# Kernel tuning notes

Measured on AMD Instinct MI355X. Metric: run time of the kernel, lower is better.

Reference implementation:

```python
import jax, jax.numpy as jnp
import numpy as np

H = 256          # decoder_size
V = 3            # vocab_size
MAX_LENGTH = 64


def lstm_cell(x, h, c, Wih, Whh, b):
    # PyTorch gate order: i, f, g, o
    g = x @ Wih.T + h @ Whh.T + b
    i, f, gg, o = jnp.split(g, 4, axis=-1)
    c = jax.nn.sigmoid(f) * c + jax.nn.sigmoid(i) * jnp.tanh(gg)
    h = jax.nn.sigmoid(o) * jnp.tanh(c)
    return h, c


def setup_inputs() -> dict:
    key = jax.random.key(0)
    ks = jax.random.split(key, 16)
    T, B, F = 512, 32, 1024
    s = 1.0 / np.sqrt(H)
    u = lambda k, shape: jax.random.uniform(k, shape, jnp.float32, -s, s)
    return dict(
        cnn_feats=jax.random.normal(ks[0], (T, B, F), jnp.float32),
        # bidirectional encoder LSTM (1 layer)
        enc_Wih_f=u(ks[1], (4 * H, F)), enc_Whh_f=u(ks[2], (4 * H, H)), enc_b_f=u(ks[3], (4 * H,)),
        enc_Wih_b=u(ks[4], (4 * H, F)), enc_Whh_b=u(ks[5], (4 * H, H)), enc_b_b=u(ks[6], (4 * H,)),
        # 2-layer decoder LSTM
        dec_Wih0=u(ks[7], (4 * H, H)), dec_Whh0=u(ks[8], (4 * H, H)), dec_b0=u(ks[9], (4 * H,)),
        dec_Wih1=u(ks[10], (4 * H, H)), dec_Whh1=u(ks[11], (4 * H, H)), dec_b1=u(ks[12], (4 * H,)),
        # per-step output projection
        lin_W=u(ks[13], (V, H)), lin_b=u(ks[14], (V,)),
    )


def _forward(cnn_feats, enc_Wih_f, enc_Whh_f, enc_b_f, enc_Wih_b, enc_Whh_b, enc_b_b,
             dec_Wih0, dec_Whh0, dec_b0, dec_Wih1, dec_Whh1, dec_b1, lin_W, lin_b):
    B = cnn_feats.shape[1]
    z = jnp.zeros((B, H), cnn_feats.dtype)

    def run_dir(seq, Wih, Whh, b):
        def step(carry, x):
            h, c = lstm_cell(x, carry[0], carry[1], Wih, Whh, b)
            return (h, c), None
        (h, c), _ = jax.lax.scan(step, (z, z), seq)
        return h, c

    # encoder final states: fwd over seq, bwd over reversed seq
    hf, cf = run_dir(cnn_feats, enc_Wih_f, enc_Whh_f, enc_b_f)
    hb, cb = run_dir(cnn_feats[::-1], enc_Wih_b, enc_Whh_b, enc_b_b)

    # decoder: layer0 init = fwd-dir state, layer1 init = bwd-dir state
    def dstep(carry, _):
        x, h0, c0, h1, c1 = carry
        h0, c0 = lstm_cell(x, h0, c0, dec_Wih0, dec_Whh0, dec_b0)
        h1, c1 = lstm_cell(h0, h1, c1, dec_Wih1, dec_Whh1, dec_b1)
        y = h1 @ lin_W.T + lin_b
        return (h1, h0, c0, h1, c1), y

    _, ys = jax.lax.scan(dstep, (z, hf, cf, hb, cb), None, length=MAX_LENGTH)
    return ys  # (MAX_LENGTH, B, V)


def reference(cnn_feats, enc_Wih_f, enc_Whh_f, enc_b_f, enc_Wih_b, enc_Whh_b, enc_b_b,
              dec_Wih0, dec_Whh0, dec_b0, dec_Wih1, dec_Whh1, dec_b1, lin_W, lin_b):
    return _forward(cnn_feats, enc_Wih_f, enc_Whh_f, enc_b_f, enc_Wih_b, enc_Whh_b, enc_b_b,
                    dec_Wih0, dec_Whh0, dec_b0, dec_Wih1, dec_Whh1, dec_b1, lin_W, lin_b)
```

## Files before the change

kernel.cpp:

```cpp
#include <hip/hip_runtime.h>
#include <stdint.h>
#include <stddef.h>

typedef __attribute__((ext_vector_type(8))) short  short8;
typedef __attribute__((ext_vector_type(4))) float  floatx4;
typedef unsigned long long u64;

#define SENT 0xAAAAAAAAAAAAAAAAull

static __device__ __forceinline__ float b2f(uint16_t h) {
  union { uint32_t u; float f; } v; v.u = ((uint32_t)h) << 16; return v.f;
}
static __device__ __forceinline__ uint16_t f2b(float f) {
  union { float f; uint32_t u; } v; v.f = f;
  uint32_t u = v.u;
  uint32_t r = u + 0x7FFFu + ((u >> 16) & 1u);
  return (uint16_t)(r >> 16);
}
static __device__ __forceinline__ float sigm(float x)  { return 1.0f / (1.0f + __expf(-x)); }
static __device__ __forceinline__ float tanh_f(float x){ return 1.0f - 2.0f / (1.0f + __expf(2.0f * x)); }

static __device__ __forceinline__ floatx4 mfma16(short8 a, short8 b, floatx4 c) {
  return __builtin_amdgcn_mfma_f32_16x16x32_bf16(a, b, c, 0, 0, 0);
}
static __device__ __forceinline__ short8 cvt8(const float* p) {
  short8 r;
  #pragma unroll
  for (int i = 0; i < 8; ++i) r[i] = (short)f2b(p[i]);
  return r;
}
static __device__ __forceinline__ u64 ld_h64(const u64* p) {
  return __hip_atomic_load(p, __ATOMIC_RELAXED, __HIP_MEMORY_SCOPE_AGENT);
}
static __device__ __forceinline__ void st_h64(uint16_t* p, u64 v) {
  __hip_atomic_store((u64*)p, v, __ATOMIC_RELAXED, __HIP_MEMORY_SCOPE_AGENT);
}
static __device__ __forceinline__ void poll8(const u64* p, u64* o) {
  for (;;) {
    bool ok = true;
    #pragma unroll
    for (int i = 0; i < 8; ++i) { o[i] = ld_h64(p + i); ok &= (o[i] != SENT); }
    if (ok) break;
    __builtin_amdgcn_s_sleep(1);
  }
}

#define H 256
#define FH 1024
#define BATCH 32
#define TSEQ 512
#define DSTEPS 64
#define ERING 8

__global__ __launch_bounds__(256) void gemm_xw(
    const float* __restrict__ A, const float* __restrict__ W,
    const float* __restrict__ bias, void* __restrict__ Cout, int out_f32)
{
  const int K = 1024, N = 1024;
  __shared__ uint16_t Ah[64 * 40], Al[64 * 40];
  __shared__ uint16_t Wh[64 * 40], Wl[64 * 40];
  const int m0 = blockIdx.x * 64;
  const int n0 = blockIdx.y * 64;
  const int tid = threadIdx.x;
  const int lane = tid & 63, w = tid >> 6;
  const int wm = w & 1, wn = w >> 1;
  const int l15 = lane & 15, q4 = lane >> 4;
  const int ldrow = tid >> 2, ldk = (tid & 3) * 8;

  floatx4 acc[2][2];
  for (int i = 0; i < 2; ++i) for (int j = 0; j < 2; ++j) acc[i][j] = (floatx4){0.f,0.f,0.f,0.f};

  for (int kb = 0; kb < K; kb += 32) {
    float aa[8], ww[8];
    {
      const float4* ap = (const float4*)(A + (size_t)(m0 + ldrow) * K + kb + ldk);
      const float4* wp = (const float4*)(W + (size_t)(n0 + ldrow) * K + kb + ldk);
      *(float4*)(aa) = ap[0]; *(float4*)(aa + 4) = ap[1];
      *(float4*)(ww) = wp[0]; *(float4*)(ww + 4) = wp[1];
    }
    short8 ah, al, wh, wl;
    #pragma unroll
    for (int i = 0; i < 8; ++i) {
      uint16_t h = f2b(aa[i]); ah[i] = (short)h; al[i] = (short)f2b(aa[i] - b2f(h));
      uint16_t g = f2b(ww[i]); wl[i] = (short)f2b(ww[i] - b2f(f2b(ww[i]) ? 0 : 0));
      wh[i] = (short)f2b(ww[i]); wl[i] = (short)f2b(ww[i] - b2f((uint16_t)wh[i]));
    }
    __syncthreads();
    *(short8*)(Ah + ldrow * 40 + ldk) = ah;
    *(short8*)(Al + ldrow * 40 + ldk) = al;
    *(short8*)(Wh + ldrow * 40 + ldk) = wh;
    *(short8*)(Wl + ldrow * 40 + ldk) = wl;
    __syncthreads();
    short8 afh[2], afl[2], bfh[2], bfl[2];
    #pragma unroll
    for (int mt = 0; mt < 2; ++mt) {
      afh[mt] = *(const short8*)(Ah + (wm * 32 + mt * 16 + l15) * 40 + q4 * 8);
      afl[mt] = *(const short8*)(Al + (wm * 32 + mt * 16 + l15) * 40 + q4 * 8);
    }
    #pragma unroll
    for (int nt = 0; nt < 2; ++nt) {
      bfh[nt] = *(const short8*)(Wh + (wn * 32 + nt * 16 + l15) * 40 + q4 * 8);
      bfl[nt] = *(const short8*)(Wl + (wn * 32 + nt * 16 + l15) * 40 + q4 * 8);
    }
    #pragma unroll
    for (int mt = 0; mt < 2; ++mt)
      #pragma unroll
      for (int nt = 0; nt < 2; ++nt) {
        acc[mt][nt] = mfma16(afh[mt], bfh[nt], acc[mt][nt]);
        acc[mt][nt] = mfma16(afh[mt], bfl[nt], acc[mt][nt]);
        acc[mt][nt] = mfma16(afl[mt], bfh[nt], acc[mt][nt]);
      }
  }
  #pragma unroll
  for (int mt = 0; mt < 2; ++mt)
    #pragma unroll
    for (int nt = 0; nt < 2; ++nt) {
      const int col = n0 + wn * 32 + nt * 16 + l15;
      const float bv = bias[col];
      #pragma unroll
      for (int r = 0; r < 4; ++r) {
        const int row = m0 + wm * 32 + mt * 16 + q4 * 4 + r;
        const float v = acc[mt][nt][r] + bv;
        if (out_f32) ((float*)Cout)[(size_t)row * N + col] = v;
        else         ((uint16_t*)Cout)[(size_t)row * N + col] = f2b(v);
      }
    }
}

__global__ __launch_bounds__(256, 1) void enc_rnn(
    const void* __restrict__ XgF, const void* __restrict__ XgB, int xg_f32,
    const float* __restrict__ WhhF, const float* __restrict__ WhhB,
    uint16_t* __restrict__ hslots,
    uint16_t* __restrict__ hfin, float* __restrict__ cfin)
{
  const int d = blockIdx.x >> 3, q = blockIdx.x & 7;
  const void*  Xg  = d ? XgB : XgF;
  const float* Whh = d ? WhhB : WhhF;
  uint16_t* hsl = hslots + d * (ERING * BATCH * H);
  const int jOff = q * 32;
  const int tid = threadIdx.x, lane = tid & 63, w = tid >> 6;
  const int tt = w & 1, nt = w >> 1, l15 = lane & 15, q4 = lane >> 4;
  const int b = nt * 16 + l15;
  const int jg = jOff + tt * 16 + q4 * 4;

  __shared__ uint16_t hS[2][32 * 264];
  __shared__ float    xgS[2][32 * 132];

  short8 Af[4][8];
  #pragma unroll
  for (int g = 0; g < 4; ++g) {
    const int grow = g * H + jOff + tt * 16 + l15;
    #pragma unroll
    for (int ks = 0; ks < 8; ++ks)
      Af[g][ks] = cvt8(Whh + (size_t)grow * H + ks * 32 + q4 * 8);
  }
  for (int i = tid; i < 32 * 264; i += 256) hS[0][i] = 0;

  float cc[4] = {0.f, 0.f, 0.f, 0.f};
  union HV { uint16_t u16[4]; u64 v; } hv; hv.v = 0ull;
  const int rb = tid >> 3, seg = tid & 7;
  const int cp = seg * 16;
  const int gge = cp >> 5, jj = cp & 31;

  for (int s = 0; s < TSEQ; ++s) {
    const int t = d ? (TSEQ - 1 - s) : s;
    const int p = s & 1;
    float xv[16];
    {
      const size_t base = (size_t)(t * BATCH + rb) * FH + gge * H + jOff + jj;
      if (xg_f32) {
        const float4* xs = (const float4*)((const float*)Xg + base);
        *(float4*)(xv) = xs[0]; *(float4*)(xv + 4) = xs[1];
        *(float4*)(xv + 8) = xs[2]; *(float4*)(xv + 12) = xs[3];
      } else {
        const uint16_t* xs = (const uint16_t*)Xg + base;
        #pragma unroll
        for (int i = 0; i < 16; ++i) xv[i] = b2f(xs[i]);
      }
    }

    if (s > 0) {
      u64 tmp[8];
      const u64* ps = (const u64*)(hsl + ((s - 1) & (ERING - 1)) * (BATCH * H) + rb * H + seg * 32);
      poll8(ps, tmp);
      #pragma unroll
      for (int i = 0; i < 8; ++i)
        *(u64*)(hS[p] + rb * 264 + seg * 32 + i * 4) = tmp[i];
    }
    if (s >= 2)
      st_h64(hsl + ((s - 2) & (ERING - 1)) * (BATCH * H) + b * H + jg, SENT);
    #pragma unroll
    for (int i = 0; i < 16; ++i) xgS[p][rb * 132 + cp + i] = xv[i];
    __syncthreads();

    floatx4 a0 = {0.f,0.f,0.f,0.f}, a1 = a0, a2 = a0, a3 = a0;
    #pragma unroll
    for (int ks = 0; ks < 8; ++ks) {
      short8 bfv = *(const short8*)(hS[p] + b * 264 + ks * 32 + q4 * 8);
      a0 = mfma16(Af[0][ks], bfv, a0);
      a1 = mfma16(Af[1][ks], bfv, a1);
      a2 = mfma16(Af[2][ks], bfv, a2);
      a3 = mfma16(Af[3][ks], bfv, a3);
    }
    #pragma unroll
    for (int r = 0; r < 4; ++r) {
      const int jl = tt * 16 + q4 * 4 + r;
      const float gi = a0[r] + xgS[p][b * 132 +      jl];
      const float gf = a1[r] + xgS[p][b * 132 + 32 + jl];
      const float gc = a2[r] + xgS[p][b * 132 + 64 + jl];
      const float go = a3[r] + xgS[p][b * 132 + 96 + jl];
      const float cn2 = sigm(gf) * cc[r] + sigm(gi) * tanh_f(gc);
      cc[r] = cn2;
      hv.u16[r] = f2b(sigm(go) * tanh_f(cn2));
    }
    st_h64(hsl + (s & (ERING - 1)) * (BATCH * H) + b * H + jg, hv.v);
  }
  #pragma unroll
  for (int r = 0; r < 4; ++r) {
    hfin[d * (BATCH * H) + b * H + jg + r] = hv.u16[r];
    cfin[d * (BATCH * H) + b * H + jg + r] = cc[r];
  }
}

__global__ __launch_bounds__(256, 1) void dec_rnn(
    const float* __restrict__ Wih0, const float* __restrict__ Whh0, const float* __restrict__ bb0,
    const float* __restrict__ Wih1, const float* __restrict__ Whh1, const float* __restrict__ bb1,
    const uint16_t* __restrict__ hfin, const float* __restrict__ cfin,
    uint16_t* __restrict__ h0slots,
    uint16_t* __restrict__ h1slots,
    float*    __restrict__ h1f)
{
  const int L = blockIdx.x >> 3, q = blockIdx.x & 7;
  const float* Wih = L ? Wih1 : Wih0;
  const float* Whh = L ? Whh1 : Whh0;
  const float* bs  = L ? bb1 : bb0;
  const int jOff = q * 32;
  const int tid = threadIdx.x, lane = tid & 63, w = tid >> 6;
  const int tt = w & 1, nt = w >> 1, l15 = lane & 15, q4 = lane >> 4;
  const int b = nt * 16 + l15;
  const int jg = jOff + tt * 16 + q4 * 4;

  __shared__ uint16_t xhS[2][32 * 528];

  short8 Af[4][16];
  #pragma unroll
  for (int g = 0; g < 4; ++g) {
    const int grow = g * H + jOff + tt * 16 + l15;
    #pragma unroll
    for (int ks = 0; ks < 8; ++ks) {
      Af[g][ks]     = cvt8(Wih + (size_t)grow * H + ks * 32 + q4 * 8);
      Af[g][8 + ks] = cvt8(Whh + (size_t)grow * H + ks * 32 + q4 * 8);
    }
  }
  float brg[4][4];
  #pragma unroll
  for (int g = 0; g < 4; ++g)
    #pragma unroll
    for (int r = 0; r < 4; ++r)
      brg[g][r] = bs[g * H + jOff + tt * 16 + q4 * 4 + r];

  float cc[4];
  #pragma unroll
  for (int r = 0; r < 4; ++r) cc[r] = cfin[L * (BATCH * H) + b * H + jg + r];

  const int rb = tid >> 3, seg = tid & 7;
  const size_t off = (size_t)rb * H + seg * 32;
  union HV { uint16_t u16[4]; u64 v; } hv; hv.v = 0ull;

  for (int t = 0; t < DSTEPS; ++t) {
    const int p = t & 1;
    u64 tx[8], th[8];
    if (t == 0) {
      const u64* ph = (const u64*)(hfin + L * (BATCH * H) + off);
      #pragma unroll
      for (int i = 0; i < 8; ++i) th[i] = ph[i];
    } else {
      const uint16_t* hb = (L ? h1slots : h0slots) + (size_t)(t - 1) * (BATCH * H);
      poll8((const u64*)(hb + off), th);
    }
    if (L == 0) {
      if (t == 0) {
        #pragma unroll
        for (int i = 0; i < 8; ++i) tx[i] = 0ull;
      } else {
        poll8((const u64*)(h1slots + (size_t)(t - 1) * (BATCH * H) + off), tx);
      }
    } else {
      poll8((const u64*)(h0slots + (size_t)t * (BATCH * H) + off), tx);
    }
    #pragma unroll
    for (int i = 0; i < 8; ++i) {
      *(u64*)(xhS[p] + rb * 528 + seg * 32 + i * 4) = tx[i];
      *(u64*)(xhS[p] + rb * 528 + 256 + seg * 32 + i * 4) = th[i];
    }
    __syncthreads();

    floatx4 a0 = {0.f,0.f,0.f,0.f}, a1 = a0, a2 = a0, a3 = a0;
    #pragma unroll
    for (int ks = 0; ks < 16; ++ks) {
      short8 bfv = *(const short8*)(xhS[p] + b * 528 + ks * 32 + q4 * 8);
      a0 = mfma16(Af[0][ks], bfv, a0);
      a1 = mfma16(Af[1][ks], bfv, a1);
      a2 = mfma16(Af[2][ks], bfv, a2);
      a3 = mfma16(Af[3][ks], bfv, a3);
    }
    float hval[4];
    #pragma unroll
    for (int r = 0; r < 4; ++r) {
      const float gi = a0[r] + brg[0][r];
      const float gf = a1[r] + brg[1][r];
      const float gc = a2[r] + brg[2][r];
      const float go = a3[r] + brg[3][r];
      const float cn2 = sigm(gf) * cc[r] + sigm(gi) * tanh_f(gc);
      cc[r] = cn2;
      hval[r] = sigm(go) * tanh_f(cn2);
      hv.u16[r] = f2b(hval[r]);
    }
    st_h64((L ? h1slots : h0slots) + (size_t)t * (BATCH * H) + b * H + jg, hv.v);
    if (L == 1) {
      float* df = h1f + (size_t)t * (BATCH * H) + b * H + jg;
      #pragma unroll
      for (int r = 0; r < 4; ++r) df[r] = hval[r];
    }
  }
}

__global__ __launch_bounds__(256) void out_proj(
    const float* __restrict__ h1f, const float* __restrict__ linW,
    const float* __restrict__ linb, float* __restrict__ out)
{
  const int idx = blockIdx.x * 256 + threadIdx.x;
  if (idx >= DSTEPS * BATCH * 3) return;
  const int v = idx % 3;
  const int tb = idx / 3;
  const float* hrow = h1f + (size_t)tb * H;
  const float* wrow = linW + (size_t)v * H;
  float s = linb[v];
  for (int k = 0; k < H; ++k) s += hrow[k] * wrow[k];
  out[idx] = s;
}

extern "C" void kernel_launch(void* const* d_in, const int* in_sizes, int n_in,
                              void* d_out, int out_size, void* d_ws, size_t ws_size,
                              hipStream_t stream) {
  (void)in_sizes; (void)n_in; (void)out_size;
  const float* cnn   = (const float*)d_in[0];
  const float* WihF  = (const float*)d_in[1];
  const float* WhhF  = (const float*)d_in[2];
  const float* bF    = (const float*)d_in[3];
  const float* WihB  = (const float*)d_in[4];
  const float* WhhB  = (const float*)d_in[5];
  const float* bB    = (const float*)d_in[6];
  const float* Wih0  = (const float*)d_in[7];
  const float* Whh0  = (const float*)d_in[8];
  const float* b0    = (const float*)d_in[9];
  const float* Wih1  = (const float*)d_in[10];
  const float* Whh1  = (const float*)d_in[11];
  const float* b1    = (const float*)d_in[12];
  const float* linW  = (const float*)d_in[13];
  const float* linb  = (const float*)d_in[14];

  const size_t XG_ELEMS = (size_t)TSEQ * BATCH * FH;
  const size_t SMALL = 2457600;
  const int xg_f32 = (ws_size >= 2 * XG_ELEMS * 4 + SMALL) ? 1 : 0;
  const size_t S = XG_ELEMS * (xg_f32 ? 4 : 2);

  uint8_t* ws = (uint8_t*)d_ws;
  void*     XgF    = (void*)(ws);
  void*     XgB    = (void*)(ws + S);
  float*    h1f    = (float*)(ws + S);
  uint8_t*  base   = ws + 2 * S;
  uint16_t* hslotsE = (uint16_t*)(base);
  uint16_t* h0slots = (uint16_t*)(base + 262144);
  uint16_t* h1slots = (uint16_t*)(base + 1310720);
  uint16_t* hfin    = (uint16_t*)(base + 2359296);
  float*    cfin    = (float*)(base + 2392064);

  hipMemsetAsync(base, 0xAA, 2359296, stream);

  gemm_xw<<<dim3(256, 16), 256, 0, stream>>>(cnn, WihF, bF, XgF, xg_f32);
  gemm_xw<<<dim3(256, 16), 256, 0, stream>>>(cnn, WihB, bB, XgB, xg_f32);
  enc_rnn<<<16, 256, 0, stream>>>(XgF, XgB, xg_f32, WhhF, WhhB,
                                  hslotsE, hfin, cfin);
  dec_rnn<<<16, 256, 0, stream>>>(Wih0, Whh0, b0, Wih1, Whh1, b1,
                                  hfin, cfin, h0slots, h1slots, h1f);
  out_proj<<<24, 256, 0, stream>>>(h1f, linW, linb, (float*)d_out);
}
```

Before: 2.589 ms.

## Co-locate recurrent blocks on one XCD and poll dual fast/slow h slots

```diff
diff --git a/kernel.cpp b/kernel.cpp
--- a/kernel.cpp
+++ b/kernel.cpp
@@ -4,6 +4,7 @@
 
 typedef __attribute__((ext_vector_type(8))) short  short8;
 typedef __attribute__((ext_vector_type(4))) float  floatx4;
+typedef __attribute__((ext_vector_type(4))) unsigned int uintx4;
 typedef unsigned long long u64;
 
 #define SENT 0xAAAAAAAAAAAAAAAAull
@@ -35,12 +36,45 @@
 static __device__ __forceinline__ void st_h64(uint16_t* p, u64 v) {
   __hip_atomic_store((u64*)p, v, __ATOMIC_RELAXED, __HIP_MEMORY_SCOPE_AGENT);
 }
-static __device__ __forceinline__ void poll8(const u64* p, u64* o) {
+static __device__ __forceinline__ void st64_sc0(uint16_t* p, u64 v) {
+  asm volatile("global_store_dwordx2 %0, %1, off sc0" : : "v"(p), "v"(v) : "memory");
+}
+static __device__ __forceinline__ void ld8_sc0(const u64* p, u64* o) {
+  uintx4 a, b, c, d;
+  asm volatile(
+    "global_load_dwordx4 %0, %4, off sc0\n\t"
+    "global_load_dwordx4 %1, %5, off sc0\n\t"
+    "global_load_dwordx4 %2, %6, off sc0\n\t"
+    "global_load_dwordx4 %3, %7, off sc0\n\t"
+    "s_waitcnt vmcnt(0)"
+    : "=&v"(a), "=&v"(b), "=&v"(c), "=&v"(d)
+    : "v"(p), "v"(p + 2), "v"(p + 4), "v"(p + 6)
+    : "memory");
+  o[0] = ((u64)a.y << 32) | a.x;  o[1] = ((u64)a.w << 32) | a.z;
+  o[2] = ((u64)b.y << 32) | b.x;  o[3] = ((u64)b.w << 32) | b.z;
+  o[4] = ((u64)c.y << 32) | c.x;  o[5] = ((u64)c.w << 32) | c.z;
+  o[6] = ((u64)d.y << 32) | d.x;  o[7] = ((u64)d.w << 32) | d.z;
+}
+static __device__ __forceinline__ void poll8_dual(const u64* pf, const u64* ps, u64* o) {
+  #pragma unroll
+  for (int i = 0; i < 8; ++i) o[i] = SENT;
   for (;;) {
+    u64 f[8];
+    ld8_sc0(pf, f);
     bool ok = true;
     #pragma unroll
-    for (int i = 0; i < 8; ++i) { o[i] = ld_h64(p + i); ok &= (o[i] != SENT); }
-    if (ok) break;
+    for (int i = 0; i < 8; ++i) {
+      if (o[i] == SENT) o[i] = f[i];
+      ok &= (o[i] != SENT);
+    }
+    if (ok) return;
+    ok = true;
+    #pragma unroll
+    for (int i = 0; i < 8; ++i) {
+      if (o[i] == SENT) o[i] = ld_h64(ps + i);
+      ok &= (o[i] != SENT);
+    }
+    if (ok) return;
     __builtin_amdgcn_s_sleep(1);
   }
 }
@@ -82,8 +116,7 @@
     #pragma unroll
     for (int i = 0; i < 8; ++i) {
       uint16_t h = f2b(aa[i]); ah[i] = (short)h; al[i] = (short)f2b(aa[i] - b2f(h));
-      uint16_t g = f2b(ww[i]); wl[i] = (short)f2b(ww[i] - b2f(f2b(ww[i]) ? 0 : 0));
-      wh[i] = (short)f2b(ww[i]); wl[i] = (short)f2b(ww[i] - b2f((uint16_t)wh[i]));
+      uint16_t g = f2b(ww[i]); wh[i] = (short)g; wl[i] = (short)f2b(ww[i] - b2f(g));
     }
     __syncthreads();
     *(short8*)(Ah + ldrow * 40 + ldk) = ah;
@@ -130,13 +163,17 @@
 __global__ __launch_bounds__(256, 1) void enc_rnn(
     const void* __restrict__ XgF, const void* __restrict__ XgB, int xg_f32,
     const float* __restrict__ WhhF, const float* __restrict__ WhhB,
-    uint16_t* __restrict__ hslots,
+    uint16_t* __restrict__ hslF,
+    uint16_t* __restrict__ hslS,
     uint16_t* __restrict__ hfin, float* __restrict__ cfin)
 {
-  const int d = blockIdx.x >> 3, q = blockIdx.x & 7;
+  const int res = blockIdx.x & 7, k = blockIdx.x >> 3;
+  if (res >= 2 || k >= 8) return;
+  const int d = res, q = k;
   const void*  Xg  = d ? XgB : XgF;
   const float* Whh = d ? WhhB : WhhF;
-  uint16_t* hsl = hslots + d * (ERING * BATCH * H);
+  uint16_t* hf = hslF + d * (ERING * BATCH * H);
+  uint16_t* hs = hslS + d * (ERING * BATCH * H);
   const int jOff = q * 32;
   const int tid = threadIdx.x, lane = tid & 63, w = tid >> 6;
   const int tt = w & 1, nt = w >> 1, l15 = lane & 15, q4 = lane >> 4;
@@ -181,14 +218,17 @@
 
     if (s > 0) {
       u64 tmp[8];
-      const u64* ps = (const u64*)(hsl + ((s - 1) & (ERING - 1)) * (BATCH * H) + rb * H + seg * 32);
-      poll8(ps, tmp);
+      const size_t soff = (size_t)((s - 1) & (ERING - 1)) * (BATCH * H) + rb * H + seg * 32;
+      poll8_dual((const u64*)(hf + soff), (const u64*)(hs + soff), tmp);
       #pragma unroll
       for (int i = 0; i < 8; ++i)
         *(u64*)(hS[p] + rb * 264 + seg * 32 + i * 4) = tmp[i];
     }
-    if (s >= 2)
-      st_h64(hsl + ((s - 2) & (ERING - 1)) * (BATCH * H) + b * H + jg, SENT);
+    if (s >= 2) {
+      const size_t poff = (size_t)((s - 2) & (ERING - 1)) * (BATCH * H) + b * H + jg;
+      st64_sc0(hf + poff, SENT);
+      st_h64(hs + poff, SENT);
+    }
     #pragma unroll
     for (int i = 0; i < 16; ++i) xgS[p][rb * 132 + cp + i] = xv[i];
     __syncthreads();
@@ -213,7 +253,9 @@
       cc[r] = cn2;
       hv.u16[r] = f2b(sigm(go) * tanh_f(cn2));
     }
-    st_h64(hsl + (s & (ERING - 1)) * (BATCH * H) + b * H + jg, hv.v);
+    const size_t woff = (size_t)(s & (ERING - 1)) * (BATCH * H) + b * H + jg;
+    st64_sc0(hf + woff, hv.v);
+    st_h64(hs + woff, hv.v);
   }
   #pragma unroll
   for (int r = 0; r < 4; ++r) {
@@ -226,11 +268,13 @@
     const float* __restrict__ Wih0, const float* __restrict__ Whh0, const float* __restrict__ bb0,
     const float* __restrict__ Wih1, const float* __restrict__ Whh1, const float* __restrict__ bb1,
     const uint16_t* __restrict__ hfin, const float* __restrict__ cfin,
-    uint16_t* __restrict__ h0slots,
-    uint16_t* __restrict__ h1slots,
+    uint16_t* __restrict__ h0F, uint16_t* __restrict__ h0S,
+    uint16_t* __restrict__ h1F, uint16_t* __restrict__ h1S,
     float*    __restrict__ h1f)
 {
-  const int L = blockIdx.x >> 3, q = blockIdx.x & 7;
+  const int res = blockIdx.x & 7, k = blockIdx.x >> 3;
+  if (res != 0 || k >= 16) return;
+  const int L = k >> 3, q = k & 7;
   const float* Wih = L ? Wih1 : Wih0;
   const float* Whh = L ? Whh1 : Whh0;
   const float* bs  = L ? bb1 : bb0;
@@ -275,18 +319,21 @@
       #pragma unroll
       for (int i = 0; i < 8; ++i) th[i] = ph[i];
     } else {
-      const uint16_t* hb = (L ? h1slots : h0slots) + (size_t)(t - 1) * (BATCH * H);
-      poll8((const u64*)(hb + off), th);
+      const size_t so = (size_t)(t - 1) * (BATCH * H) + off;
+      poll8_dual((const u64*)((L ? h1F : h0F) + so),
+                 (const u64*)((L ? h1S : h0S) + so), th);
     }
     if (L == 0) {
       if (t == 0) {
         #pragma unroll
         for (int i = 0; i < 8; ++i) tx[i] = 0ull;
       } else {
-        poll8((const u64*)(h1slots + (size_t)(t - 1) * (BATCH * H) + off), tx);
+        const size_t so = (size_t)(t - 1) * (BATCH * H) + off;
+        poll8_dual((const u64*)(h1F + so), (const u64*)(h1S + so), tx);
       }
     } else {
-      poll8((const u64*)(h0slots + (size_t)t * (BATCH * H) + off), tx);
+      const size_t so = (size_t)t * (BATCH * H) + off;
+      poll8_dual((const u64*)(h0F + so), (const u64*)(h0S + so), tx);
     }
     #pragma unroll
     for (int i = 0; i < 8; ++i) {
@@ -316,7 +363,9 @@
       hval[r] = sigm(go) * tanh_f(cn2);
       hv.u16[r] = f2b(hval[r]);
     }
-    st_h64((L ? h1slots : h0slots) + (size_t)t * (BATCH * H) + b * H + jg, hv.v);
+    const size_t wo = (size_t)t * (BATCH * H) + b * H + jg;
+    st64_sc0((L ? h1F : h0F) + wo, hv.v);
+    st_h64((L ? h1S : h0S) + wo, hv.v);
     if (L == 1) {
       float* df = h1f + (size_t)t * (BATCH * H) + b * H + jg;
       #pragma unroll
@@ -361,7 +410,7 @@
   const float* linb  = (const float*)d_in[14];
 
   const size_t XG_ELEMS = (size_t)TSEQ * BATCH * FH;
-  const size_t SMALL = 2457600;
+  const size_t SMALL = 622592;
   const int xg_f32 = (ws_size >= 2 * XG_ELEMS * 4 + SMALL) ? 1 : 0;
   const size_t S = XG_ELEMS * (xg_f32 ? 4 : 2);
 
@@ -370,19 +419,23 @@
   void*     XgB    = (void*)(ws + S);
   float*    h1f    = (float*)(ws + S);
   uint8_t*  base   = ws + 2 * S;
-  uint16_t* hslotsE = (uint16_t*)(base);
-  uint16_t* h0slots = (uint16_t*)(base + 262144);
-  uint16_t* h1slots = (uint16_t*)(base + 1310720);
-  uint16_t* hfin    = (uint16_t*)(base + 2359296);
-  float*    cfin    = (float*)(base + 2392064);
-
-  hipMemsetAsync(base, 0xAA, 2359296, stream);
+  uint16_t* hslF   = (uint16_t*)(base);
+  uint16_t* hslS   = (uint16_t*)(base + 262144);
+  uint16_t* hfin   = (uint16_t*)(base + 524288);
+  float*    cfin   = (float*)(base + 557056);
+  uint16_t* h0F = (uint16_t*)(ws);
+  uint16_t* h0S = (uint16_t*)(ws + 1048576);
+  uint16_t* h1F = (uint16_t*)(ws + 2097152);
+  uint16_t* h1S = (uint16_t*)(ws + 3145728);
+
+  hipMemsetAsync(base, 0xAA, 524288, stream);
 
   gemm_xw<<<dim3(256, 16), 256, 0, stream>>>(cnn, WihF, bF, XgF, xg_f32);
   gemm_xw<<<dim3(256, 16), 256, 0, stream>>>(cnn, WihB, bB, XgB, xg_f32);
-  enc_rnn<<<16, 256, 0, stream>>>(XgF, XgB, xg_f32, WhhF, WhhB,
-                                  hslotsE, hfin, cfin);
-  dec_rnn<<<16, 256, 0, stream>>>(Wih0, Whh0, b0, Wih1, Whh1, b1,
-                                  hfin, cfin, h0slots, h1slots, h1f);
+  enc_rnn<<<128, 256, 0, stream>>>(XgF, XgB, xg_f32, WhhF, WhhB,
+                                   hslF, hslS, hfin, cfin);
+  hipMemsetAsync(ws, 0xAA, 4194304, stream);
+  dec_rnn<<<128, 256, 0, stream>>>(Wih0, Whh0, b0, Wih1, Whh1, b1,
+                                   hfin, cfin, h0F, h0S, h1F, h1S, h1f);
   out_proj<<<24, 256, 0, stream>>>(h1f, linW, linb, (float*)d_out);
 }
```

New measurement: 3.230 ms. 24.8% more time.

## Prefetch next-step encoder gate inputs and merge decoder dual-slot polling

Applied to the files above, without the earlier changes.

```diff
diff --git a/kernel.cpp b/kernel.cpp
--- a/kernel.cpp
+++ b/kernel.cpp
@@ -82,8 +82,7 @@
     #pragma unroll
     for (int i = 0; i < 8; ++i) {
       uint16_t h = f2b(aa[i]); ah[i] = (short)h; al[i] = (short)f2b(aa[i] - b2f(h));
-      uint16_t g = f2b(ww[i]); wl[i] = (short)f2b(ww[i] - b2f(f2b(ww[i]) ? 0 : 0));
-      wh[i] = (short)f2b(ww[i]); wl[i] = (short)f2b(ww[i] - b2f((uint16_t)wh[i]));
+      uint16_t g = f2b(ww[i]); wh[i] = (short)g; wl[i] = (short)f2b(ww[i] - b2f(g));
     }
     __syncthreads();
     *(short8*)(Ah + ldrow * 40 + ldk) = ah;
@@ -162,22 +161,25 @@
   const int cp = seg * 16;
   const int gge = cp >> 5, jj = cp & 31;
 
+  float xv[16], xn[16];
+  #define LOAD_XG(dst, s_) do {                                              \
+    const int t_ = d ? (TSEQ - 1 - (s_)) : (s_);                             \
+    const size_t base_ = (size_t)(t_ * BATCH + rb) * FH + gge * H + jOff + jj;\
+    if (xg_f32) {                                                            \
+      const float4* xs_ = (const float4*)((const float*)Xg + base_);         \
+      *(float4*)(dst) = xs_[0]; *(float4*)((dst) + 4) = xs_[1];              \
+      *(float4*)((dst) + 8) = xs_[2]; *(float4*)((dst) + 12) = xs_[3];       \
+    } else {                                                                 \
+      const uint16_t* xs_ = (const uint16_t*)Xg + base_;                     \
+      _Pragma("unroll")                                                      \
+      for (int i_ = 0; i_ < 16; ++i_) (dst)[i_] = b2f(xs_[i_]);              \
+    }                                                                        \
+  } while (0)
+
+  LOAD_XG(xv, 0);
+
   for (int s = 0; s < TSEQ; ++s) {
-    const int t = d ? (TSEQ - 1 - s) : s;
     const int p = s & 1;
-    float xv[16];
-    {
-      const size_t base = (size_t)(t * BATCH + rb) * FH + gge * H + jOff + jj;
-      if (xg_f32) {
-        const float4* xs = (const float4*)((const float*)Xg + base);
-        *(float4*)(xv) = xs[0]; *(float4*)(xv + 4) = xs[1];
-        *(float4*)(xv + 8) = xs[2]; *(float4*)(xv + 12) = xs[3];
-      } else {
-        const uint16_t* xs = (const uint16_t*)Xg + base;
-        #pragma unroll
-        for (int i = 0; i < 16; ++i) xv[i] = b2f(xs[i]);
-      }
-    }
 
     if (s > 0) {
       u64 tmp[8];
@@ -191,6 +193,7 @@
       st_h64(hsl + ((s - 2) & (ERING - 1)) * (BATCH * H) + b * H + jg, SENT);
     #pragma unroll
     for (int i = 0; i < 16; ++i) xgS[p][rb * 132 + cp + i] = xv[i];
+    if (s + 1 < TSEQ) LOAD_XG(xn, s + 1);
     __syncthreads();
 
     floatx4 a0 = {0.f,0.f,0.f,0.f}, a1 = a0, a2 = a0, a3 = a0;
@@ -214,12 +217,15 @@
       hv.u16[r] = f2b(sigm(go) * tanh_f(cn2));
     }
     st_h64(hsl + (s & (ERING - 1)) * (BATCH * H) + b * H + jg, hv.v);
+    #pragma unroll
+    for (int i = 0; i < 16; ++i) xv[i] = xn[i];
   }
   #pragma unroll
   for (int r = 0; r < 4; ++r) {
     hfin[d * (BATCH * H) + b * H + jg + r] = hv.u16[r];
     cfin[d * (BATCH * H) + b * H + jg + r] = cc[r];
   }
+  #undef LOAD_XG
 }
 
 __global__ __launch_bounds__(256, 1) void dec_rnn(
@@ -270,23 +276,45 @@
   for (int t = 0; t < DSTEPS; ++t) {
     const int p = t & 1;
     u64 tx[8], th[8];
+    const u64* pa = nullptr;
+    const u64* pb = nullptr;
     if (t == 0) {
       const u64* ph = (const u64*)(hfin + L * (BATCH * H) + off);
-      #pragma unroll
       for (int i = 0; i < 8; ++i) th[i] = ph[i];
     } else {
-      const uint16_t* hb = (L ? h1slots : h0slots) + (size_t)(t - 1) * (BATCH * H);
-      poll8((const u64*)(hb + off), th);
+      pa = (const u64*)(((L ? h1slots : h0slots) + (size_t)(t - 1) * (BATCH * H)) + off);
     }
     if (L == 0) {
       if (t == 0) {
-        #pragma unroll
         for (int i = 0; i < 8; ++i) tx[i] = 0ull;
       } else {
-        poll8((const u64*)(h1slots + (size_t)(t - 1) * (BATCH * H) + off), tx);
+        pb = (const u64*)(h1slots + (size_t)(t - 1) * (BATCH * H) + off);
       }
     } else {
-      poll8((const u64*)(h0slots + (size_t)t * (BATCH * H) + off), tx);
+      pb = (const u64*)(h0slots + (size_t)t * (BATCH * H) + off);
+    }
+    if (pa || pb) {
+      if (pa) { for (int i = 0; i < 8; ++i) th[i] = SENT; }
+      if (pb) { for (int i = 0; i < 8; ++i) tx[i] = SENT; }
+      for (;;) {
+        bool ok = true;
+        if (pa) {
+          #pragma unroll
+          for (int i = 0; i < 8; ++i) {
+            if (th[i] == SENT) th[i] = ld_h64(pa + i);
+            ok &= (th[i] != SENT);
+          }
+        }
+        if (pb) {
+          #pragma unroll
+          for (int i = 0; i < 8; ++i) {
+            if (tx[i] == SENT) tx[i] = ld_h64(pb + i);
+            ok &= (tx[i] != SENT);
+          }
+        }
+        if (ok) break;
+        __builtin_amdgcn_s_sleep(1);
+      }
     }
     #pragma unroll
     for (int i = 0; i < 8; ++i) {
@@ -376,7 +404,7 @@
   uint16_t* hfin    = (uint16_t*)(base + 2359296);
   float*    cfin    = (float*)(base + 2392064);
 
-  hipMemsetAsync(base, 0xAA, 2359296, stream);
+  (void)hipMemsetAsync(base, 0xAA, 2359296, stream);
 
   gemm_xw<<<dim3(256, 16), 256, 0, stream>>>(cnn, WihF, bF, XgF, xg_f32);
   gemm_xw<<<dim3(256, 16), 256, 0, stream>>>(cnn, WihB, bB, XgB, xg_f32);
```

Measured after the change: 2.620 ms. No clear change (+1.2%).
